# Performance work log

Hardware: AMD Instinct MI355X
Metric: run time of the kernel (lower is better)

The kernel has to match this reference:

```python
import jax, jax.numpy as jnp
import numpy as np

N, C, H, DH = 4096, 256, 8, 32
E = 32768
MAX_SPD = 3
DEG_B = 8
LN_EPS = 1e-5


def _ln(h, g, b):
    mu = jnp.mean(h, axis=-1, keepdims=True)
    var = jnp.mean((h - mu) ** 2, axis=-1, keepdims=True)
    return g * (h - mu) / jnp.sqrt(var + LN_EPS) + b


def setup_inputs() -> dict:
    key = jax.random.key(0)
    ks = jax.random.split(key, 16)
    s = 1.0 / np.sqrt(C).astype(np.float32)
    s4 = 1.0 / np.sqrt(4 * C).astype(np.float32)
    return {
        "x": jax.random.normal(ks[0], (N, C), jnp.float32),
        "edge_index": jax.random.randint(ks[1], (2, E), 0, N, dtype=jnp.int32),
        "Wq": jax.random.normal(ks[2], (C, C), jnp.float32) * s,
        "bq": jnp.zeros((C,), jnp.float32),
        "Wk": jax.random.normal(ks[3], (C, C), jnp.float32) * s,
        "bk": jnp.zeros((C,), jnp.float32),
        "Wv": jax.random.normal(ks[4], (C, C), jnp.float32) * s,
        "bv": jnp.zeros((C,), jnp.float32),
        "Wo": jax.random.normal(ks[5], (C, C), jnp.float32) * s,
        "bo": jnp.zeros((C,), jnp.float32),
        "W1": jax.random.normal(ks[6], (C, 4 * C), jnp.float32) * s,
        "b1": jnp.zeros((4 * C,), jnp.float32),
        "W2": jax.random.normal(ks[7], (4 * C, C), jnp.float32) * s4,
        "b2": jnp.zeros((C,), jnp.float32),
        "g1": jnp.ones((C,), jnp.float32),
        "beta1": jnp.zeros((C,), jnp.float32),
        "g2": jnp.ones((C,), jnp.float32),
        "beta2": jnp.zeros((C,), jnp.float32),
        # spd_emb is zero-init in torch; use small random so the bias path is exercised
        "spd_emb": jax.random.normal(ks[8], (MAX_SPD + 2, H), jnp.float32) * 0.02,
        "in_deg_emb": jax.random.normal(ks[9], (DEG_B + 1, C), jnp.float32) * 0.02,
        "out_deg_emb": jax.random.normal(ks[10], (DEG_B + 1, C), jnp.float32) * 0.02,
        "et_bias": jax.random.normal(ks[11], (), jnp.float32) * 0.02,
    }


def _bucket(d):
    # floor(log2(d+1)) clamped to [0, DEG_B]
    return jnp.clip(jnp.floor(jnp.log2(d + 1.0)), 0, DEG_B).astype(jnp.int32)


def _spd_buckets(src, dst):
    # use_reverse_spd=True: adjacency A[row=dst, col=src]; anchors = dst, probe = src.
    # Frontier F starts as identity over all nodes (superset of unique-anchor columns;
    # extra columns never probed -> identical result to torch's unique-anchor version).
    F = jnp.eye(N, dtype=jnp.float32)
    spd = jnp.full((E,), MAX_SPD + 1, dtype=jnp.int32)
    unset = jnp.ones((E,), dtype=bool)
    for k in range(1, MAX_SPD + 1):
        # (A @ F) > 0  via edge-gather + per-row max (binary reachability)
        F = (jax.ops.segment_max(F[src], dst, num_segments=N) > 0).astype(jnp.float32)
        reach = F[src, dst] > 0  # probe anchor column dst at row src
        newly = unset & reach
        spd = jnp.where(newly, k, spd)
        unset = unset & ~newly
    return jnp.clip(spd, 1, MAX_SPD + 1)


def reference(x, edge_index, Wq, bq, Wk, bk, Wv, bv, Wo, bo, W1, b1, W2, b2,
              g1, beta1, g2, beta2, spd_emb, in_deg_emb, out_deg_emb, et_bias):
    src, dst = edge_index[0], edge_index[1]
    ones = jnp.ones((E,), jnp.float32)
    in_deg = jax.ops.segment_sum(ones, dst, num_segments=N)
    out_deg = jax.ops.segment_sum(ones, src, num_segments=N)
    x_in = x + in_deg_emb[_bucket(in_deg)] + out_deg_emb[_bucket(out_deg)]

    spd = _spd_buckets(src, dst)  # [E] int in [1, MAX_SPD+1]

    xn = _ln(x_in, g1, beta1)
    Q = (xn @ Wq + bq).reshape(N, H, DH)
    K = (xn @ Wk + bk).reshape(N, H, DH)
    V = (xn @ Wv + bv).reshape(N, H, DH)

    scores = jnp.sum(Q[dst] * K[src], axis=-1) / np.sqrt(DH)  # [E, H]
    scores = scores + spd_emb[spd] + et_bias

    # segment softmax over edges sharing a destination node
    m = jax.ops.segment_max(scores, dst, num_segments=N)  # [N, H]
    m = jnp.where(jnp.isfinite(m), m, 0.0)
    e = jnp.exp(scores - m[dst])
    ssum = jax.ops.segment_sum(e, dst, num_segments=N)
    w = e / jnp.where(ssum[dst] > 0, ssum[dst], 1.0)  # [E, H]

    msg = jax.ops.segment_sum(w[:, :, None] * V[src], dst, num_segments=N)  # [N,H,DH]
    h = x_in + msg.reshape(N, C) @ Wo + bo
    hn = _ln(h, g2, beta2)
    ff = jax.nn.gelu(hn @ W1 + b1, approximate=False) @ W2 + b2
    return h + ff
```

## Files before the change

### kernel.cpp

```cpp
#include <hip/hip_runtime.h>
#include <math.h>

#define NN 4096
#define CC 256
#define HH 8
#define DHD 32
#define EE 32768
#define FW 128
#define MAXD 64

typedef float f32x4 __attribute__((ext_vector_type(4)));
typedef __bf16 bf16x8 __attribute__((ext_vector_type(8)));
typedef __bf16 bf16x4 __attribute__((ext_vector_type(4)));

__device__ __forceinline__ int bucketf(int d){
  float l = log2f((float)d + 1.0f);
  int b = (int)floorf(l);
  return b < 0 ? 0 : (b > 8 ? 8 : b);
}

__global__ void k_scatter(const int* __restrict__ src, const int* __restrict__ dst,
                          int* __restrict__ cursor, int* __restrict__ outdeg,
                          int* __restrict__ nsrc){
  int e = blockIdx.x*256+threadIdx.x;
  if(e<EE){
    int d = dst[e], s = src[e];
    atomicAdd(&outdeg[s],1);
    int p = atomicAdd(&cursor[d],1);
    if(p < MAXD) nsrc[d*MAXD+p] = s;
  }
}

__global__ void k_mid(const int* __restrict__ cursor, const int* __restrict__ nsrc,
                      unsigned* __restrict__ F1,
                      const float* __restrict__ x,
                      const int* __restrict__ outdeg, const float* __restrict__ iemb,
                      const float* __restrict__ oemb, const float* __restrict__ g,
                      const float* __restrict__ be, float* __restrict__ x_in,
                      __bf16* __restrict__ xn){
  int b = blockIdx.x;
  int tid = threadIdx.x;
  if(b < 2048){
    int d = b*2 + (tid>>7);
    int w = tid & 127;
    int cdeg = cursor[d]; if(cdeg > MAXD) cdeg = MAXD;
    const int* row = nsrc + d*MAXD;
    unsigned v = 0;
    for(int i=0;i<cdeg;i++){
      int s = row[i];
      if((s>>5) == w) v |= 1u << (s&31);
    }
    F1[(size_t)d*FW + w] = v;
    return;
  }
  int node = (b-2048)*4 + (tid >> 6);
  int lane = tid & 63;
  int bi = bucketf(cursor[node]);
  int bo = bucketf(outdeg[node]);
  float4 xv = ((const float4*)(x + (size_t)node*CC))[lane];
  float4 iv = ((const float4*)(iemb + (size_t)bi*CC))[lane];
  float4 ov = ((const float4*)(oemb + (size_t)bo*CC))[lane];
  float4 v;
  v.x = xv.x+iv.x+ov.x; v.y = xv.y+iv.y+ov.y;
  v.z = xv.z+iv.z+ov.z; v.w = xv.w+iv.w+ov.w;
  ((float4*)(x_in + (size_t)node*CC))[lane] = v;
  float s  = v.x+v.y+v.z+v.w;
  float sq = v.x*v.x+v.y*v.y+v.z*v.z+v.w*v.w;
  #pragma unroll
  for(int m=32;m>=1;m>>=1){ s += __shfl_xor(s,m); sq += __shfl_xor(sq,m); }
  float mu  = s * (1.0f/CC);
  float var = sq * (1.0f/CC) - mu*mu;
  float inv = rsqrtf(var + 1e-5f);
  float4 gv = ((const float4*)g)[lane];
  float4 bv = ((const float4*)be)[lane];
  bf16x4 o;
  o[0] = (__bf16)(gv.x*(v.x-mu)*inv + bv.x);
  o[1] = (__bf16)(gv.y*(v.y-mu)*inv + bv.y);
  o[2] = (__bf16)(gv.z*(v.z-mu)*inv + bv.z);
  o[3] = (__bf16)(gv.w*(v.w-mu)*inv + bv.w);
  *(bf16x4*)(xn + (size_t)node*CC + lane*4) = o;
}

__global__ void k_prop(const int* __restrict__ cursor, const int* __restrict__ nsrc,
                       const unsigned* __restrict__ Fin, unsigned* __restrict__ Fout){
  int d = blockIdx.x; int w = threadIdx.x;
  int cdeg = cursor[d]; if(cdeg > MAXD) cdeg = MAXD;
  const int* row = nsrc + d*MAXD;
  unsigned v = 0;
  for(int i=0;i<cdeg;i++){
    v |= Fin[(size_t)row[i]*FW + w];
  }
  Fout[(size_t)d*FW + w] = v;
}

__global__ void k_ln(const float* __restrict__ in, const float* __restrict__ g,
                     const float* __restrict__ b, __bf16* __restrict__ out){
  int node = blockIdx.x*4 + (threadIdx.x >> 6);
  int lane = threadIdx.x & 63;
  float4 v = ((const float4*)(in + (size_t)node*CC))[lane];
  float s  = v.x+v.y+v.z+v.w;
  float sq = v.x*v.x+v.y*v.y+v.z*v.z+v.w*v.w;
  #pragma unroll
  for(int m=32;m>=1;m>>=1){ s += __shfl_xor(s,m); sq += __shfl_xor(sq,m); }
  float mu  = s * (1.0f/CC);
  float var = sq * (1.0f/CC) - mu*mu;
  float inv = rsqrtf(var + 1e-5f);
  float4 gv = ((const float4*)g)[lane];
  float4 bv = ((const float4*)b)[lane];
  bf16x4 o;
  o[0] = (__bf16)(gv.x*(v.x-mu)*inv + bv.x);
  o[1] = (__bf16)(gv.y*(v.y-mu)*inv + bv.y);
  o[2] = (__bf16)(gv.z*(v.z-mu)*inv + bv.z);
  o[3] = (__bf16)(gv.w*(v.w-mu)*inv + bv.w);
  *(bf16x4*)(out + (size_t)node*CC + lane*4) = o;
}

__global__ void k_pre(const float* __restrict__ Wq, const float* __restrict__ Wk,
                      const float* __restrict__ Wv, const float* __restrict__ Wo,
                      const float* __restrict__ W1, const float* __restrict__ W2,
                      const float* __restrict__ bq, const float* __restrict__ bk,
                      const float* __restrict__ bv,
                      __bf16* __restrict__ WqkvT, __bf16* __restrict__ WoT,
                      __bf16* __restrict__ W1T, __bf16* __restrict__ W2T,
                      float* __restrict__ bqkv, int* __restrict__ zero_base){
  int b = blockIdx.x;
  int tid = threadIdx.x;
  if(b >= 193){
    zero_base[(b-193)*256 + tid] = 0;
    return;
  }
  if(b == 192){
    bqkv[tid]     = bq[tid];
    bqkv[256+tid] = bk[tid];
    bqkv[512+tid] = bv[tid];
    return;
  }
  const float* W; __bf16* Wt; int K, N, tile;
  if(b < 16)      { W=Wq; Wt=WqkvT;        K=256;  N=256;  tile=b; }
  else if(b < 32) { W=Wk; Wt=WqkvT+65536;  K=256;  N=256;  tile=b-16; }
  else if(b < 48) { W=Wv; Wt=WqkvT+131072; K=256;  N=256;  tile=b-32; }
  else if(b < 64) { W=Wo; Wt=WoT;          K=256;  N=256;  tile=b-48; }
  else if(b < 128){ W=W1; Wt=W1T;          K=256;  N=1024; tile=b-64; }
  else            { W=W2; Wt=W2T;          K=1024; N=256;  tile=b-128; }
  int nK = K/64;
  int tk = tile % nK, tn = tile / nK;
  __shared__ float T[64][65];
  int c = tid & 63, r0 = tid >> 6;
  #pragma unroll
  for(int i=0;i<16;i++){
    int row = r0*16 + i;
    T[row][c] = W[(size_t)(tk*64+row)*N + tn*64 + c];
  }
  __syncthreads();
  #pragma unroll
  for(int i=0;i<16;i++){
    int row = r0*16 + i;
    Wt[(size_t)(tn*64+row)*K + tk*64 + c] = (__bf16)T[c][row];
  }
}

template<int MODE>
__global__ __launch_bounds__(256) void k_bgemm(const __bf16* __restrict__ A, const __bf16* __restrict__ Bt,
                       const float* __restrict__ bias, const float* __restrict__ add,
                       float* __restrict__ outf, __bf16* __restrict__ outb,
                       int M, int N, int K){
  __shared__ __bf16 As[64*64];
  __shared__ __bf16 Bs[64*64];
  const int tid = threadIdx.x;
  const int lane = tid & 63;
  const int w = tid >> 6;
  const int wr = w >> 1, wc = w & 1;
  const int l15 = lane & 15, g = lane >> 4;
  const int bm = blockIdx.y*64, bn = blockIdx.x*64;
  f32x4 acc[2][2] = {};
  for(int k0=0; k0<K; k0+=64){
    #pragma unroll
    for(int rep=0; rep<2; rep++){
      int q = tid + rep*256;
      int row = q>>3;
      int scb = ((q&7)*16) ^ ((row&7)<<4);
      const __bf16* srcA = A  + (size_t)(bm+row)*K + k0 + (scb>>1);
      const __bf16* srcB = Bt + (size_t)(bn+row)*K + k0 + (scb>>1);
      __builtin_amdgcn_global_load_lds(
        (const __attribute__((address_space(1))) void*)srcA,
        (__attribute__((address_space(3))) void*)((char*)As + q*16), 16, 0, 0);
      __builtin_amdgcn_global_load_lds(
        (const __attribute__((address_space(1))) void*)srcB,
        (__attribute__((address_space(3))) void*)((char*)Bs + q*16), 16, 0, 0);
    }
    __syncthreads();
    #pragma unroll
    for(int ks=0; ks<2; ks++){
      bf16x8 a[2], b[2];
      #pragma unroll
      for(int i=0;i<2;i++){
        int row = wr*32 + i*16 + l15;
        int byte_ = row*128 + ks*64 + g*16; byte_ ^= (row&7)<<4;
        a[i] = *(const bf16x8*)((const char*)As + byte_);
      }
      #pragma unroll
      for(int j=0;j<2;j++){
        int row = wc*32 + j*16 + l15;
        int byte_ = row*128 + ks*64 + g*16; byte_ ^= (row&7)<<4;
        b[j] = *(const bf16x8*)((const char*)Bs + byte_);
      }
      #pragma unroll
      for(int i=0;i<2;i++)
        #pragma unroll
        for(int j=0;j<2;j++)
          acc[i][j] = __builtin_amdgcn_mfma_f32_16x16x32_bf16(a[i], b[j], acc[i][j], 0, 0, 0);
    }
    __syncthreads();
  }
  #pragma unroll
  for(int i=0;i<2;i++){
    #pragma unroll
    for(int j=0;j<2;j++){
      int col = bn + wc*32 + j*16 + l15;
      float bv = bias[col];
      #pragma unroll
      for(int r=0;r<4;r++){
        int rowg = bm + wr*32 + i*16 + g*4 + r;
        float v = acc[i][j][r] + bv;
        if(MODE==1) v += add[(size_t)rowg*N + col];
        if(MODE==2){
          v = 0.5f*v*(1.0f + erff(v*0.70710678118654752f));
          outb[(size_t)rowg*N + col] = (__bf16)v;
        } else if(MODE==3){
          outb[(size_t)rowg*N + col] = (__bf16)v;
        } else {
          outf[(size_t)rowg*N + col] = v;
        }
      }
    }
  }
}

__global__ __launch_bounds__(256) void k_pq(const int* __restrict__ cursor, const int* __restrict__ nsrc,
                    const unsigned* __restrict__ F2, unsigned* __restrict__ F3,
                    const __bf16* __restrict__ A, const __bf16* __restrict__ Bt,
                    const float* __restrict__ bias, __bf16* __restrict__ outb){
  __shared__ __bf16 As[64*64];
  __shared__ __bf16 Bs[64*64];
  const int b = blockIdx.x;
  const int tid = threadIdx.x;
  if(b < 2048){
    int d = b*2 + (tid>>7);
    int w_ = tid & 127;
    int cdeg = cursor[d]; if(cdeg > MAXD) cdeg = MAXD;
    const int* row = nsrc + d*MAXD;
    unsigned v = 0;
    for(int i=0;i<cdeg;i++) v |= F2[(size_t)row[i]*FW + w_];
    F3[(size_t)d*FW + w_] = v;
    return;
  }
  const int bx = b - 2048;
  const int N = 768, K = 256;
  const int bm = (bx/12)*64, bn = (bx%12)*64;
  const int lane = tid & 63;
  const int w = tid >> 6;
  const int wr = w >> 1, wc = w & 1;
  const int l15 = lane & 15, g = lane >> 4;
  f32x4 acc[2][2] = {};
  for(int k0=0; k0<K; k0+=64){
    #pragma unroll
    for(int rep=0; rep<2; rep++){
      int q = tid + rep*256;
      int row = q>>3;
      int scb = ((q&7)*16) ^ ((row&7)<<4);
      const __bf16* srcA = A  + (size_t)(bm+row)*K + k0 + (scb>>1);
      const __bf16* srcB = Bt + (size_t)(bn+row)*K + k0 + (scb>>1);
      __builtin_amdgcn_global_load_lds(
        (const __attribute__((address_space(1))) void*)srcA,
        (__attribute__((address_space(3))) void*)((char*)As + q*16), 16, 0, 0);
      __builtin_amdgcn_global_load_lds(
        (const __attribute__((address_space(1))) void*)srcB,
        (__attribute__((address_space(3))) void*)((char*)Bs + q*16), 16, 0, 0);
    }
    __syncthreads();
    #pragma unroll
    for(int ks=0; ks<2; ks++){
      bf16x8 a[2], bb[2];
      #pragma unroll
      for(int i=0;i<2;i++){
        int row = wr*32 + i*16 + l15;
        int byte_ = row*128 + ks*64 + g*16; byte_ ^= (row&7)<<4;
        a[i] = *(const bf16x8*)((const char*)As + byte_);
      }
      #pragma unroll
      for(int j=0;j<2;j++){
        int row = wc*32 + j*16 + l15;
        int byte_ = row*128 + ks*64 + g*16; byte_ ^= (row&7)<<4;
        bb[j] = *(const bf16x8*)((const char*)Bs + byte_);
      }
      #pragma unroll
      for(int i=0;i<2;i++)
        #pragma unroll
        for(int j=0;j<2;j++)
          acc[i][j] = __builtin_amdgcn_mfma_f32_16x16x32_bf16(a[i], bb[j], acc[i][j], 0, 0, 0);
    }
    __syncthreads();
  }
  #pragma unroll
  for(int i=0;i<2;i++){
    #pragma unroll
    for(int j=0;j<2;j++){
      int col = bn + wc*32 + j*16 + l15;
      float bv = bias[col];
      #pragma unroll
      for(int r=0;r<4;r++){
        int rowg = bm + wr*32 + i*16 + g*4 + r;
        outb[(size_t)rowg*N + col] = (__bf16)(acc[i][j][r] + bv);
      }
    }
  }
}

__global__ void k_sagg(const int* __restrict__ nsrc, const int* __restrict__ cursor,
                       const __bf16* __restrict__ QKV,
                       const unsigned* __restrict__ F1, const unsigned* __restrict__ F2,
                       const unsigned* __restrict__ F3,
                       const float* __restrict__ spde, __bf16* __restrict__ msg){
  __shared__ float scs[MAXD][9];
  __shared__ int   sl[MAXD];
  __shared__ int   spi[MAXD];
  const int d = blockIdx.x;
  const int t = threadIdx.x;
  int deg = cursor[d]; if(deg > MAXD) deg = MAXD;
  if(t < deg){
    int s = nsrc[d*MAXD+t];
    sl[t] = s;
    size_t wi = (size_t)s*FW + (d>>5); unsigned bb = 1u << (d&31);
    int sp = 4;
    if(F3[wi] & bb) sp = 3;
    if(F2[wi] & bb) sp = 2;
    if(F1[wi] & bb) sp = 1;
    spi[t] = sp;
  }
  __syncthreads();
  { const int h = t & 7, i0 = t >> 3;
    const bf16x8* qr = (const bf16x8*)(QKV + (size_t)d*768 + h*DHD);
    for(int i=i0; i<deg; i+=32){
      const bf16x8* kr = (const bf16x8*)(QKV + (size_t)sl[i]*768 + 256 + h*DHD);
      float acc = 0.f;
      #pragma unroll
      for(int j=0;j<4;j++){
        bf16x8 kv = kr[j], qv = qr[j];
        #pragma unroll
        for(int u=0;u<8;u++) acc += (float)qv[u] * (float)kv[u];
      }
      scs[i][h] = acc * 0.17677669529663687f + spde[spi[i]*HH + h];
    }
  }
  __syncthreads();
  { const int h = t >> 5, l = t & 31;
    float m = -3.0e38f;
    for(int i=l;i<deg;i+=32) m = fmaxf(m, scs[i][h]);
    #pragma unroll
    for(int mk=16;mk>=1;mk>>=1) m = fmaxf(m, __shfl_xor(m,mk));
    float ss = 0.f;
    for(int i=l;i<deg;i+=32) ss += expf(scs[i][h]-m);
    #pragma unroll
    for(int mk=16;mk>=1;mk>>=1) ss += __shfl_xor(ss,mk);
    float inv = (ss>0.f) ? 1.f/ss : 1.f;
    for(int i=l;i<deg;i+=32) scs[i][h] = expf(scs[i][h]-m)*inv;
  }
  __syncthreads();
  { const int h = t >> 5, c = t & 31;
    float acc = 0.f;
    for(int i=0;i<deg;i++)
      acc += scs[i][h] * (float)QKV[(size_t)sl[i]*768 + 512 + h*DHD + c];
    msg[(size_t)d*CC + h*DHD + c] = (__bf16)acc;
  }
}

extern "C" void kernel_launch(void* const* d_in, const int* in_sizes, int n_in,
                              void* d_out, int out_size, void* d_ws, size_t ws_size,
                              hipStream_t stream){
  const float* x  = (const float*)d_in[0];
  const int*  ei  = (const int*)d_in[1];
  const float* Wq = (const float*)d_in[2];  const float* bq = (const float*)d_in[3];
  const float* Wk = (const float*)d_in[4];  const float* bk = (const float*)d_in[5];
  const float* Wv = (const float*)d_in[6];  const float* bv = (const float*)d_in[7];
  const float* Wo = (const float*)d_in[8];  const float* bo = (const float*)d_in[9];
  const float* W1 = (const float*)d_in[10]; const float* b1 = (const float*)d_in[11];
  const float* W2 = (const float*)d_in[12]; const float* b2 = (const float*)d_in[13];
  const float* g1 = (const float*)d_in[14]; const float* be1= (const float*)d_in[15];
  const float* g2 = (const float*)d_in[16]; const float* be2= (const float*)d_in[17];
  const float* spde = (const float*)d_in[18];
  const float* iemb = (const float*)d_in[19];
  const float* oemb = (const float*)d_in[20];
  const float* etb  = (const float*)d_in[21]; (void)etb;
  const int* src = ei;
  const int* dst = ei + EE;
  float* out = (float*)d_out;

  const size_t NC = (size_t)NN*CC;
  float* ws   = (float*)d_ws;
  float* x_in = ws;
  float* hbuf = ws + NC;
  int* cursor = (int*)(ws + 2*NC);
  int* outdeg = cursor + NN;
  unsigned* F1 = (unsigned*)(ws + 2*NC + 12288);
  unsigned* F2 = F1 + (size_t)NN*FW;
  unsigned* F3 = F2 + (size_t)NN*FW;
  __bf16* QKV  = (__bf16*)(F3 + (size_t)NN*FW);
  int* nsrc    = (int*)(ws + 5255168);
  __bf16* xn_bf  = (__bf16*)(ws + 5517312);
  __bf16* msg_bf = (__bf16*)(ws + 6041600);
  __bf16* WqkvT  = (__bf16*)(ws + 6565888);
  __bf16* WoT    = WqkvT + 196608;
  __bf16* W1T    = WoT + 65536;
  __bf16* W2T    = W1T + 262144;
  float* bqkv    = ws + 6959104;
  __bf16* ff1_bf = (__bf16*)(ws + 2*NC);
  __bf16* hn_bf  = (__bf16*)(ws + 4*NC);

  k_pre<<<225,256,0,stream>>>(Wq,Wk,Wv,Wo,W1,W2,bq,bk,bv,WqkvT,WoT,W1T,W2T,bqkv,cursor);
  k_scatter<<<EE/256,256,0,stream>>>(src,dst,cursor,outdeg,nsrc);
  k_mid<<<3072,256,0,stream>>>(cursor,nsrc,F1,x,outdeg,iemb,oemb,g1,be1,x_in,xn_bf);
  k_prop<<<NN,FW,0,stream>>>(cursor,nsrc,F1,F2);
  k_pq<<<2816,256,0,stream>>>(cursor,nsrc,F2,F3,xn_bf,WqkvT,bqkv,QKV);
  k_sagg<<<NN,256,0,stream>>>(nsrc,cursor,QKV,F1,F2,F3,spde,msg_bf);
  dim3 go(256/64, NN/64);
  k_bgemm<1><<<go,256,0,stream>>>(msg_bf, WoT, bo, x_in, hbuf, nullptr, NN, 256, 256);
  k_ln <<<NN/4,256,0,stream>>>(hbuf,g2,be2,hn_bf);
  dim3 gf1(1024/64, NN/64);
  k_bgemm<2><<<gf1,256,0,stream>>>(hn_bf, W1T, b1, nullptr, nullptr, ff1_bf, NN, 1024, 256);
  dim3 gf2(256/64, NN/64);
  k_bgemm<1><<<gf2,256,0,stream>>>(ff1_bf, W2T, b2, hbuf, out, nullptr, NN, 256, 1024);
}
```

Measured before the change: 82.10 us.

## Fuse output projection GEMM with LayerNorm and split score dot products across lanes

Replaces the Wo GEMM plus separate LayerNorm launch with one kernel in which each block computes full 256-wide rows (16 rows per block), adds bias and residual, reduces mean and variance in-block, and writes both h and the bf16 normalized output. This removes one launch and a global round trip of h. In exchange only 256 blocks run and each reloads the full Wo tile. Separately, the score computation in the attention kernel now splits each 32-element dot product over 4 lanes with shuffle reduction, giving more parallelism per edge.

```diff
diff --git a/kernel.cpp b/kernel.cpp
--- a/kernel.cpp
+++ b/kernel.cpp
@@ -93,28 +93,6 @@
   Fout[(size_t)d*FW + w] = v;
 }
 
-__global__ void k_ln(const float* __restrict__ in, const float* __restrict__ g,
-                     const float* __restrict__ b, __bf16* __restrict__ out){
-  int node = blockIdx.x*4 + (threadIdx.x >> 6);
-  int lane = threadIdx.x & 63;
-  float4 v = ((const float4*)(in + (size_t)node*CC))[lane];
-  float s  = v.x+v.y+v.z+v.w;
-  float sq = v.x*v.x+v.y*v.y+v.z*v.z+v.w*v.w;
-  #pragma unroll
-  for(int m=32;m>=1;m>>=1){ s += __shfl_xor(s,m); sq += __shfl_xor(sq,m); }
-  float mu  = s * (1.0f/CC);
-  float var = sq * (1.0f/CC) - mu*mu;
-  float inv = rsqrtf(var + 1e-5f);
-  float4 gv = ((const float4*)g)[lane];
-  float4 bv = ((const float4*)b)[lane];
-  bf16x4 o;
-  o[0] = (__bf16)(gv.x*(v.x-mu)*inv + bv.x);
-  o[1] = (__bf16)(gv.y*(v.y-mu)*inv + bv.y);
-  o[2] = (__bf16)(gv.z*(v.z-mu)*inv + bv.z);
-  o[3] = (__bf16)(gv.w*(v.w-mu)*inv + bv.w);
-  *(bf16x4*)(out + (size_t)node*CC + lane*4) = o;
-}
-
 __global__ void k_pre(const float* __restrict__ Wq, const float* __restrict__ Wk,
                       const float* __restrict__ Wv, const float* __restrict__ Wo,
                       const float* __restrict__ W1, const float* __restrict__ W2,
@@ -232,6 +210,109 @@
           outf[(size_t)rowg*N + col] = v;
         }
       }
+    }
+  }
+}
+
+__global__ __launch_bounds__(256) void k_wln(const __bf16* __restrict__ A, const __bf16* __restrict__ Bt,
+                    const float* __restrict__ bias, const float* __restrict__ add,
+                    const float* __restrict__ g2, const float* __restrict__ be2,
+                    float* __restrict__ hbuf, __bf16* __restrict__ hn){
+  __shared__ __bf16 As[16*64];
+  __shared__ __bf16 Bs[256*64];
+  __shared__ float partS[64], partQ[64], muv[16], invv[16];
+  const int tid = threadIdx.x;
+  const int lane = tid & 63;
+  const int w = tid >> 6;
+  const int l15 = lane & 15, g = lane >> 4;
+  const int bm = blockIdx.x*16;
+  const int K = 256, N = 256;
+  f32x4 acc[4] = {};
+  for(int k0=0; k0<K; k0+=64){
+    if(tid < 128){
+      int q = tid;
+      int row = q>>3;
+      int scb = ((q&7)*16) ^ ((row&7)<<4);
+      const __bf16* srcA = A + (size_t)(bm+row)*K + k0 + (scb>>1);
+      __builtin_amdgcn_global_load_lds(
+        (const __attribute__((address_space(1))) void*)srcA,
+        (__attribute__((address_space(3))) void*)((char*)As + q*16), 16, 0, 0);
+    }
+    #pragma unroll
+    for(int rep=0; rep<8; rep++){
+      int q = tid + rep*256;
+      int row = q>>3;
+      int scb = ((q&7)*16) ^ ((row&7)<<4);
+      const __bf16* srcB = Bt + (size_t)row*K + k0 + (scb>>1);
+      __builtin_amdgcn_global_load_lds(
+        (const __attribute__((address_space(1))) void*)srcB,
+        (__attribute__((address_space(3))) void*)((char*)Bs + q*16), 16, 0, 0);
+    }
+    __syncthreads();
+    #pragma unroll
+    for(int ks=0; ks<2; ks++){
+      bf16x8 a, b[4];
+      { int row = l15;
+        int byte_ = row*128 + ks*64 + g*16; byte_ ^= (row&7)<<4;
+        a = *(const bf16x8*)((const char*)As + byte_); }
+      #pragma unroll
+      for(int j=0;j<4;j++){
+        int row = w*64 + j*16 + l15;
+        int byte_ = row*128 + ks*64 + g*16; byte_ ^= (row&7)<<4;
+        b[j] = *(const bf16x8*)((const char*)Bs + byte_);
+      }
+      #pragma unroll
+      for(int j=0;j<4;j++)
+        acc[j] = __builtin_amdgcn_mfma_f32_16x16x32_bf16(a, b[j], acc[j], 0, 0, 0);
+    }
+    __syncthreads();
+  }
+  float v[4][4];
+  #pragma unroll
+  for(int j=0;j<4;j++){
+    int col = w*64 + j*16 + l15;
+    float bv = bias[col];
+    #pragma unroll
+    for(int r=0;r<4;r++){
+      int rowg = bm + g*4 + r;
+      v[j][r] = acc[j][r] + bv + add[(size_t)rowg*N + col];
+    }
+  }
+  float s[4], qq[4];
+  #pragma unroll
+  for(int r=0;r<4;r++){
+    s[r] = v[0][r]+v[1][r]+v[2][r]+v[3][r];
+    qq[r] = v[0][r]*v[0][r]+v[1][r]*v[1][r]+v[2][r]*v[2][r]+v[3][r]*v[3][r];
+  }
+  #pragma unroll
+  for(int m=8;m>=1;m>>=1){
+    #pragma unroll
+    for(int r=0;r<4;r++){ s[r] += __shfl_xor(s[r],m); qq[r] += __shfl_xor(qq[r],m); }
+  }
+  if(l15==0){
+    #pragma unroll
+    for(int r=0;r<4;r++){ partS[w*16 + g*4 + r] = s[r]; partQ[w*16 + g*4 + r] = qq[r]; }
+  }
+  __syncthreads();
+  if(tid < 16){
+    float S = partS[tid] + partS[16+tid] + partS[32+tid] + partS[48+tid];
+    float Q = partQ[tid] + partQ[16+tid] + partQ[32+tid] + partQ[48+tid];
+    float mu = S * (1.0f/256.0f);
+    float var = Q * (1.0f/256.0f) - mu*mu;
+    muv[tid] = mu;
+    invv[tid] = rsqrtf(var + 1e-5f);
+  }
+  __syncthreads();
+  #pragma unroll
+  for(int j=0;j<4;j++){
+    int col = w*64 + j*16 + l15;
+    float gv = g2[col], bev = be2[col];
+    #pragma unroll
+    for(int r=0;r<4;r++){
+      int rowg = bm + g*4 + r;
+      float mu = muv[g*4+r], iv = invv[g*4+r];
+      hbuf[(size_t)rowg*N + col] = v[j][r];
+      hn[(size_t)rowg*N + col] = (__bf16)(gv*(v[j][r]-mu)*iv + bev);
     }
   }
 }
@@ -338,18 +419,16 @@
     spi[t] = sp;
   }
   __syncthreads();
-  { const int h = t & 7, i0 = t >> 3;
-    const bf16x8* qr = (const bf16x8*)(QKV + (size_t)d*768 + h*DHD);
-    for(int i=i0; i<deg; i+=32){
-      const bf16x8* kr = (const bf16x8*)(QKV + (size_t)sl[i]*768 + 256 + h*DHD);
-      float acc = 0.f;
-      #pragma unroll
-      for(int j=0;j<4;j++){
-        bf16x8 kv = kr[j], qv = qr[j];
-        #pragma unroll
-        for(int u=0;u<8;u++) acc += (float)qv[u] * (float)kv[u];
-      }
-      scs[i][h] = acc * 0.17677669529663687f + spde[spi[i]*HH + h];
+  { const int i0 = t>>5, h = (t>>2)&7, q = t&3;
+    bf16x8 qv = *(const bf16x8*)(QKV + (size_t)d*768 + h*DHD + q*8);
+    for(int i=i0; i<deg; i+=8){
+      bf16x8 kv = *(const bf16x8*)(QKV + (size_t)sl[i]*768 + 256 + h*DHD + q*8);
+      float p = 0.f;
+      #pragma unroll
+      for(int u=0;u<8;u++) p += (float)qv[u] * (float)kv[u];
+      p += __shfl_xor(p,1);
+      p += __shfl_xor(p,2);
+      if(q==0) scs[i][h] = p * 0.17677669529663687f + spde[spi[i]*HH + h];
     }
   }
   __syncthreads();
@@ -422,9 +501,7 @@
   k_prop<<<NN,FW,0,stream>>>(cursor,nsrc,F1,F2);
   k_pq<<<2816,256,0,stream>>>(cursor,nsrc,F2,F3,xn_bf,WqkvT,bqkv,QKV);
   k_sagg<<<NN,256,0,stream>>>(nsrc,cursor,QKV,F1,F2,F3,spde,msg_bf);
-  dim3 go(256/64, NN/64);
-  k_bgemm<1><<<go,256,0,stream>>>(msg_bf, WoT, bo, x_in, hbuf, nullptr, NN, 256, 256);
-  k_ln <<<NN/4,256,0,stream>>>(hbuf,g2,be2,hn_bf);
+  k_wln<<<NN/16,256,0,stream>>>(msg_bf, WoT, bo, x_in, g2, be2, hbuf, hn_bf);
   dim3 gf1(1024/64, NN/64);
   k_bgemm<2><<<gf1,256,0,stream>>>(hn_bf, W1T, b1, nullptr, nullptr, ff1_bf, NN, 1024, 256);
   dim3 gf2(256/64, NN/64);
```

Result: no change. 80.71 us (-1.7%).
